# Kernel tuning notes

Measured on AMD Instinct MI355X. Metric: run time of the kernel, lower is better.

The kernel has to match this reference:

```python
import jax, jax.numpy as jnp
import numpy as np

B, N, H = 128, 1024, 128          # graphs, nodes per graph, hidden size
K1, K2, K3 = 512, 256, 128        # ceil(ratio^l * N), ratio = 0.5
DEG = 8                           # avg degree
E = B * N * DEG                   # total edges (fixed, masked after pooling)


def gcn_conv(x, row, col, mask, W, b, n):
    h = x @ W
    deg = jax.ops.segment_sum(mask, col, num_segments=n) + 1.0  # + self loop
    dinv = jax.lax.rsqrt(deg)
    coef = (dinv[row] * dinv[col] * mask)[:, None]
    agg = jax.ops.segment_sum(h[row] * coef, col, num_segments=n)
    return agg + h * (dinv * dinv)[:, None] + b  # self-loop term + bias


def topk_pool(x, row, col, mask, p, n_graphs, n_per, k):
    # PyG TopKPooling: y = x.p/||p||, keep per-graph top-k, x' = x[perm]*tanh(y[perm])
    score = (x @ p) / jnp.linalg.norm(p)
    vals, idx = jax.lax.top_k(score.reshape(n_graphs, n_per), k)  # [B, k]
    sel = (idx + (jnp.arange(n_graphs) * n_per)[:, None]).reshape(-1)
    xs = x[sel] * jnp.tanh(vals.reshape(-1))[:, None]
    # relabel edges; drop edges touching removed nodes via mask
    newid = jnp.full((n_graphs * n_per,), -1, jnp.int32).at[sel].set(
        jnp.arange(n_graphs * k, dtype=jnp.int32))
    nr, nc = newid[row], newid[col]
    nmask = mask * ((nr >= 0) & (nc >= 0)).astype(mask.dtype)
    return xs, jnp.maximum(nr, 0), jnp.maximum(nc, 0), nmask


def readout(x, n_graphs, k):
    # cat([gmp, gap]) with contiguous equal-size graphs
    xg = x.reshape(n_graphs, k, -1)
    return jnp.concatenate([xg.max(axis=1), xg.mean(axis=1)], axis=1)


def _forward(x, edge_row, edge_col, W1, b1, p1, W2, b2, p2, W3, b3, p3):
    mask = jnp.ones((E,), x.dtype)
    h = jax.nn.relu(gcn_conv(x, edge_row, edge_col, mask, W1, b1, B * N))
    x1, r, c, m = topk_pool(h, edge_row, edge_col, mask, p1, B, N, K1)
    out = readout(x1, B, K1)
    h = jax.nn.relu(gcn_conv(x1, r, c, m, W2, b2, B * K1))
    x2, r, c, m = topk_pool(h, r, c, m, p2, B, K1, K2)
    out = out + readout(x2, B, K2)
    h = jax.nn.relu(gcn_conv(x2, r, c, m, W3, b3, B * K2))
    x3, r, c, m = topk_pool(h, r, c, m, p3, B, K2, K3)
    out = out + readout(x3, B, K3)
    return out  # [B, 2*H]


def setup_inputs() -> dict:
    key = jax.random.key(0)
    ks = jax.random.split(key, 12)
    x = jax.random.normal(ks[0], (B * N, H), jnp.float32)
    off = (jnp.arange(B, dtype=jnp.int32) * N)[:, None]
    edge_row = (jax.random.randint(ks[1], (B, N * DEG), 0, N, jnp.int32) + off).reshape(-1)
    edge_col = (jax.random.randint(ks[2], (B, N * DEG), 0, N, jnp.int32) + off).reshape(-1)
    s = 1.0 / np.sqrt(H)
    params = {}
    for i, tag in enumerate(["1", "2", "3"]):
        params["W" + tag] = jax.random.normal(ks[3 + 3 * i], (H, H), jnp.float32) * s
        params["b" + tag] = jnp.zeros((H,), jnp.float32)
        params["p" + tag] = jax.random.normal(ks[4 + 3 * i], (H,), jnp.float32)
    return {"x": x, "edge_row": edge_row, "edge_col": edge_col, **params}


def reference(x, edge_row, edge_col, W1, b1, p1, W2, b2, p2, W3, b3, p3):
    return _forward(x, edge_row, edge_col, W1, b1, p1, W2, b2, p2, W3, b3, p3)
```

## Files before the change

### kernel.cpp

```cpp
#include <hip/hip_runtime.h>
#include <math.h>

#define BG   128
#define NPER 1024
#define HDIM 128
#define NEDGE (BG * NPER * 8)
#define NMAX (BG * NPER)
#define EPG  (NEDGE / BG)
#define CAP  48
#define PRE  16

typedef __attribute__((ext_vector_type(8))) short s16x8;
typedef __attribute__((ext_vector_type(4))) float f32x4;

static __device__ __forceinline__ ushort f2bf(float f) {
  uint u = __float_as_uint(f);
  return (ushort)((u + 0x7fffu + ((u >> 16) & 1u)) >> 16);
}
static __device__ __forceinline__ float bf2f(ushort h) {
  return __uint_as_float(((uint)h) << 16);
}

extern __shared__ float ldsbuf[];


__global__ __launch_bounds__(1024) void countfill_lds_kernel(
    const int* __restrict__ cr, const int* __restrict__ cc,
    int* __restrict__ cnt, int* __restrict__ meta8,
    int* __restrict__ srcext, int* __restrict__ order,
    int* __restrict__ odeg) {
  int* smeta = (int*)ldsbuf;
  int* scnt  = smeta + NPER * PRE;
  int* sbb   = scnt + NPER;
  int g = blockIdx.x, t = threadIdx.x;
  scnt[t] = 0;
  if (t < 2) sbb[t] = 0;
  __syncthreads();

  const int4* cr4 = (const int4*)(cr + (size_t)g * EPG);
  const int4* cc4 = (const int4*)(cc + (size_t)g * EPG);
  #pragma unroll
  for (int i = 0; i < 2; ++i) {
    int4 r = cr4[t * 2 + i];
    int4 c = cc4[t * 2 + i];
    int rl, cl, pos;
    cl = c.x & (NPER - 1); rl = r.x & (NPER - 1);
    pos = atomicAdd(&scnt[cl], 1);
    if (pos < PRE) smeta[cl * PRE + pos] = rl;
    else if (pos < CAP) srcext[((size_t)g * NPER + cl) * CAP + pos] = rl;
    cl = c.y & (NPER - 1); rl = r.y & (NPER - 1);
    pos = atomicAdd(&scnt[cl], 1);
    if (pos < PRE) smeta[cl * PRE + pos] = rl;
    else if (pos < CAP) srcext[((size_t)g * NPER + cl) * CAP + pos] = rl;
    cl = c.z & (NPER - 1); rl = r.z & (NPER - 1);
    pos = atomicAdd(&scnt[cl], 1);
    if (pos < PRE) smeta[cl * PRE + pos] = rl;
    else if (pos < CAP) srcext[((size_t)g * NPER + cl) * CAP + pos] = rl;
    cl = c.w & (NPER - 1); rl = r.w & (NPER - 1);
    pos = atomicAdd(&scnt[cl], 1);
    if (pos < PRE) smeta[cl * PRE + pos] = rl;
    else if (pos < CAP) srcext[((size_t)g * NPER + cl) * CAP + pos] = rl;
  }
  __syncthreads();

  int4* mo = (int4*)(meta8 + (size_t)g * NPER * PRE);
  const int4* sm4 = (const int4*)smeta;
  #pragma unroll
  for (int i = 0; i < 4; ++i) mo[i * 1024 + t] = sm4[i * 1024 + t];
  int d = scnt[t];
  cnt[g * NPER + t] = d;

  int bkt = d > 8 ? 1 : 0;
  int bpos = atomicAdd(&sbb[bkt], 1);
  __syncthreads();
  int slot = bkt ? sbb[0] + bpos : bpos;
  order[g * NPER + slot] = t;
  odeg[g * NPER + slot] = d;
}


__global__ __launch_bounds__(1024) void agg_lds_kernel(
    const float* __restrict__ x, float* __restrict__ z,
    const int* __restrict__ meta8, const int* __restrict__ srcext,
    const int* __restrict__ deg, const int* __restrict__ order,
    const int* __restrict__ odeg, int npg) {
  float* sX = ldsbuf;
  float* sDinv = sX + npg * 32;
  int g = blockIdx.x >> 2;
  int chunk = blockIdx.x & 3;
  int t = threadIdx.x;
  int base = g * npg;

  const float4* x4 = (const float4*)x;
  float4* sX4 = (float4*)sX;
  for (int i = t; i < npg * 8; i += 1024) {
    int r = i >> 3, l8 = i & 7;
    float dv = rsqrtf((float)deg[base + r] + 1.0f);
    float4 v = x4[(size_t)(base + r) * 32 + chunk * 8 + l8];
    v.x *= dv; v.y *= dv; v.z *= dv; v.w *= dv;
    sX4[i] = v;
  }
  for (int i = t; i < npg; i += 1024)
    sDinv[i] = rsqrtf((float)deg[base + i] + 1.0f);

  int dl = t >> 3, l = t & 7;
  const int4* m4 = (const int4*)meta8;
  float4* z4 = (float4*)z;

  int ordc = order[base + dl];
  int dpc  = odeg[base + dl];
  int ordn = order[base + dl + 128];
  int dpn  = odeg[base + dl + 128];
  int4 c0 = m4[(size_t)(base + ordc) * 4 + 0];
  int4 c1 = m4[(size_t)(base + ordc) * 4 + 1];
  int4 c2 = {0, 0, 0, 0}, c3 = {0, 0, 0, 0};
  if (dpc > 8) {
    c2 = m4[(size_t)(base + ordc) * 4 + 2];
    c3 = m4[(size_t)(base + ordc) * 4 + 3];
  }

  __syncthreads();

  for (int slot = dl; slot < npg; slot += 128) {
    int ordn2 = ordn, dpn2 = dpn;
    if (slot + 256 < npg) {
      ordn2 = order[base + slot + 256];
      dpn2  = odeg[base + slot + 256];
    }
    int4 n0 = {0,0,0,0}, n1 = {0,0,0,0}, n2 = {0,0,0,0}, n3 = {0,0,0,0};
    if (slot + 128 < npg) {
      n0 = m4[(size_t)(base + ordn) * 4 + 0];
      n1 = m4[(size_t)(base + ordn) * 4 + 1];
      if (dpn > 8) {
        n2 = m4[(size_t)(base + ordn) * 4 + 2];
        n3 = m4[(size_t)(base + ordn) * 4 + 3];
      }
    }

    int dst = ordc;
    int node = base + dst;
    int d = dpc > CAP ? CAP : dpc;
    int dp = d > PRE ? PRE : d;
    float dc = sDinv[dst];

    int sA0 = (0 < dp) ? c0.x : dst;
    int sA1 = (1 < dp) ? c0.y : dst;
    int sA2 = (2 < dp) ? c0.z : dst;
    int sA3 = (3 < dp) ? c0.w : dst;
    int sA4 = (4 < dp) ? c1.x : dst;
    int sA5 = (5 < dp) ? c1.y : dst;
    int sA6 = (6 < dp) ? c1.z : dst;
    int sA7 = (7 < dp) ? c1.w : dst;
    float4 w  = sX4[dst * 8 + l];
    float4 p0 = sX4[sA0 * 8 + l];
    float4 p1 = sX4[sA1 * 8 + l];
    float4 p2 = sX4[sA2 * 8 + l];
    float4 p3 = sX4[sA3 * 8 + l];
    float4 p4 = sX4[sA4 * 8 + l];
    float4 p5 = sX4[sA5 * 8 + l];
    float4 p6 = sX4[sA6 * 8 + l];
    float4 p7 = sX4[sA7 * 8 + l];
    float4 a0, a1, a2, a3;
    a0.x = w.x + p0.x; a0.y = w.y + p0.y; a0.z = w.z + p0.z; a0.w = w.w + p0.w;
    a1.x = p1.x + p5.x; a1.y = p1.y + p5.y; a1.z = p1.z + p5.z; a1.w = p1.w + p5.w;
    a2.x = p2.x + p6.x; a2.y = p2.y + p6.y; a2.z = p2.z + p6.z; a2.w = p2.w + p6.w;
    a3.x = p3.x + p7.x; a3.y = p3.y + p7.y; a3.z = p3.z + p7.z; a3.w = p3.w + p7.w;
    a0.x += p4.x; a0.y += p4.y; a0.z += p4.z; a0.w += p4.w;

    int nslots = 8;
    if (dp > 8) {
      int sB0 = (8 < dp)  ? c2.x : dst;
      int sB1 = (9 < dp)  ? c2.y : dst;
      int sB2 = (10 < dp) ? c2.z : dst;
      int sB3 = (11 < dp) ? c2.w : dst;
      int sB4 = (12 < dp) ? c3.x : dst;
      int sB5 = (13 < dp) ? c3.y : dst;
      int sB6 = (14 < dp) ? c3.z : dst;
      int sB7 = (15 < dp) ? c3.w : dst;
      float4 q0 = sX4[sB0 * 8 + l];
      float4 q1 = sX4[sB1 * 8 + l];
      float4 q2 = sX4[sB2 * 8 + l];
      float4 q3 = sX4[sB3 * 8 + l];
      float4 q4 = sX4[sB4 * 8 + l];
      float4 q5 = sX4[sB5 * 8 + l];
      float4 q6 = sX4[sB6 * 8 + l];
      float4 q7 = sX4[sB7 * 8 + l];
      a0.x += q0.x; a0.y += q0.y; a0.z += q0.z; a0.w += q0.w;
      a1.x += q1.x; a1.y += q1.y; a1.z += q1.z; a1.w += q1.w;
      a2.x += q2.x; a2.y += q2.y; a2.z += q2.z; a2.w += q2.w;
      a3.x += q3.x; a3.y += q3.y; a3.z += q3.z; a3.w += q3.w;
      a0.x += q4.x; a0.y += q4.y; a0.z += q4.z; a0.w += q4.w;
      a1.x += q5.x; a1.y += q5.y; a1.z += q5.z; a1.w += q5.w;
      a2.x += q6.x; a2.y += q6.y; a2.z += q6.z; a2.w += q6.w;
      a3.x += q7.x; a3.y += q7.y; a3.z += q7.z; a3.w += q7.w;
      nslots = 16;
    }

    if (d > PRE) {
      for (int e2 = PRE; e2 < d; ++e2) {
        int rl = srcext[(size_t)node * CAP + e2];
        float4 v0 = sX4[rl * 8 + l];
        a0.x += v0.x; a0.y += v0.y; a0.z += v0.z; a0.w += v0.w;
      }
    }

    float corr = (float)(nslots - dp);
    float4 o;
    o.x = (a0.x + a1.x + a2.x + a3.x - corr * w.x) * dc;
    o.y = (a0.y + a1.y + a2.y + a3.y - corr * w.y) * dc;
    o.z = (a0.z + a1.z + a2.z + a3.z - corr * w.z) * dc;
    o.w = (a0.w + a1.w + a2.w + a3.w - corr * w.w) * dc;
    z4[(size_t)node * 32 + chunk * 8 + l] = o;

    ordc = ordn; dpc = dpn; ordn = ordn2; dpn = dpn2;
    c0 = n0; c1 = n1; c2 = n2; c3 = n3;
  }
}


__global__ __launch_bounds__(256) void wsplit_kernel(
    const float* __restrict__ W0, const float* __restrict__ W1,
    const float* __restrict__ W2, ushort* __restrict__ wpk) {
  int id = blockIdx.x * 256 + threadIdx.x;
  int L = id >> 14;
  int r = id & 16383;
  int i = r & 7;
  int lane = (r >> 3) & 63;
  int nt = (r >> 9) & 7;
  int kt = (r >> 12) & 3;
  int k = kt * 32 + (lane >> 4) * 8 + i;
  int n = nt * 16 + (lane & 15);
  const float* W = (L == 0) ? W0 : (L == 1) ? W1 : W2;
  float v = W[k * HDIM + n];
  ushort h = f2bf(v);
  float r1 = v - bf2f(h);
  ushort m = f2bf(r1);
  ushort lo = f2bf(r1 - bf2f(m));
  size_t base = (size_t)L * 3 * 16384 + (size_t)r;
  wpk[base] = h;
  wpk[base + 16384] = m;
  wpk[base + 32768] = lo;
}


__global__ __launch_bounds__(256, 2) void conv_mfma_kernel(
    float* __restrict__ zh, const ushort* __restrict__ wpk,
    const float* __restrict__ bias, const float* __restrict__ p,
    float* __restrict__ score) {
  int t = threadIdx.x;
  int wv = t >> 6, l = t & 63;
  int lr = l & 15, lq = l >> 4;
  int arowA = blockIdx.x * 128 + wv * 16 + lr;
  int arowB = arowA + 64;
  const float* zrowA = zh + (size_t)arowA * HDIM + lq * 8;
  const float* zrowB = zh + (size_t)arowB * HDIM + lq * 8;

  s16x8 ahA[4], amA[4], alA[4], ahB[4], amB[4], alB[4];
  #pragma unroll
  for (int kt = 0; kt < 4; ++kt) {
    float4 v0 = ((const float4*)(zrowA + kt * 32))[0];
    float4 v1 = ((const float4*)(zrowA + kt * 32))[1];
    float fA[8] = {v0.x, v0.y, v0.z, v0.w, v1.x, v1.y, v1.z, v1.w};
    float4 u0 = ((const float4*)(zrowB + kt * 32))[0];
    float4 u1 = ((const float4*)(zrowB + kt * 32))[1];
    float fB[8] = {u0.x, u0.y, u0.z, u0.w, u1.x, u1.y, u1.z, u1.w};
    #pragma unroll
    for (int i = 0; i < 8; ++i) {
      ushort h = f2bf(fA[i]);
      float r1 = fA[i] - bf2f(h);
      ushort m = f2bf(r1);
      ushort lo = f2bf(r1 - bf2f(m));
      ahA[kt][i] = (short)h; amA[kt][i] = (short)m; alA[kt][i] = (short)lo;
      h = f2bf(fB[i]);
      r1 = fB[i] - bf2f(h);
      m = f2bf(r1);
      lo = f2bf(r1 - bf2f(m));
      ahB[kt][i] = (short)h; amB[kt][i] = (short)m; alB[kt][i] = (short)lo;
    }
  }

  f32x4 accA[8], accB[8];
  #pragma unroll
  for (int nt = 0; nt < 8; ++nt) { accA[nt] = (f32x4)(0.f); accB[nt] = (f32x4)(0.f); }

  const s16x8* wh = (const s16x8*)wpk;
  const s16x8* wm = wh + 2048;
  const s16x8* wl = wm + 2048;

  #pragma unroll
  for (int kt = 0; kt < 4; ++kt) {
    #pragma unroll
    for (int nt = 0; nt < 8; ++nt) {
      int fi = (kt * 8 + nt) * 64 + l;
      s16x8 bh = wh[fi];
      s16x8 bm = wm[fi];
      s16x8 bl = wl[fi];
      accA[nt] = __builtin_amdgcn_mfma_f32_16x16x32_bf16(ahA[kt], bh, accA[nt], 0, 0, 0);
      accA[nt] = __builtin_amdgcn_mfma_f32_16x16x32_bf16(ahA[kt], bm, accA[nt], 0, 0, 0);
      accA[nt] = __builtin_amdgcn_mfma_f32_16x16x32_bf16(amA[kt], bh, accA[nt], 0, 0, 0);
      accA[nt] = __builtin_amdgcn_mfma_f32_16x16x32_bf16(ahA[kt], bl, accA[nt], 0, 0, 0);
      accA[nt] = __builtin_amdgcn_mfma_f32_16x16x32_bf16(alA[kt], bh, accA[nt], 0, 0, 0);
      accA[nt] = __builtin_amdgcn_mfma_f32_16x16x32_bf16(amA[kt], bm, accA[nt], 0, 0, 0);
      accB[nt] = __builtin_amdgcn_mfma_f32_16x16x32_bf16(ahB[kt], bh, accB[nt], 0, 0, 0);
      accB[nt] = __builtin_amdgcn_mfma_f32_16x16x32_bf16(ahB[kt], bm, accB[nt], 0, 0, 0);
      accB[nt] = __builtin_amdgcn_mfma_f32_16x16x32_bf16(amB[kt], bh, accB[nt], 0, 0, 0);
      accB[nt] = __builtin_amdgcn_mfma_f32_16x16x32_bf16(ahB[kt], bl, accB[nt], 0, 0, 0);
      accB[nt] = __builtin_amdgcn_mfma_f32_16x16x32_bf16(alB[kt], bh, accB[nt], 0, 0, 0);
      accB[nt] = __builtin_amdgcn_mfma_f32_16x16x32_bf16(amB[kt], bm, accB[nt], 0, 0, 0);
    }
  }

  int orowA = blockIdx.x * 128 + wv * 16 + lq * 4;
  int orowB = orowA + 64;
  float partA[4] = {0.f, 0.f, 0.f, 0.f};
  float partB[4] = {0.f, 0.f, 0.f, 0.f};
  #pragma unroll
  for (int nt = 0; nt < 8; ++nt) {
    float bv = bias[nt * 16 + lr];
    float pv = p[nt * 16 + lr];
    #pragma unroll
    for (int j = 0; j < 4; ++j) {
      float hA = fmaxf(accA[nt][j] + bv, 0.f);
      partA[j] += hA * pv;
      zh[(size_t)(orowA + j) * HDIM + nt * 16 + lr] = hA;
      float hB = fmaxf(accB[nt][j] + bv, 0.f);
      partB[j] += hB * pv;
      zh[(size_t)(orowB + j) * HDIM + nt * 16 + lr] = hB;
    }
  }
  #pragma unroll
  for (int j = 0; j < 4; ++j) {
    #pragma unroll
    for (int s = 1; s < 16; s <<= 1) {
      partA[j] += __shfl_xor(partA[j], s);
      partB[j] += __shfl_xor(partB[j], s);
    }
    if (lr == 0) {
      score[orowA + j] = partA[j];
      score[orowB + j] = partB[j];
    }
  }
}


__global__ __launch_bounds__(1024) void topk_mega_kernel(
    const float* __restrict__ score, const float* __restrict__ p,
    const float* __restrict__ h, float* __restrict__ xo,
    const int* __restrict__ in_r, const int* __restrict__ in_c,
    int* __restrict__ out_r, int* __restrict__ out_c,
    int* __restrict__ meta8, int* __restrict__ srcext,
    int* __restrict__ cnt, float* __restrict__ acc,
    int* __restrict__ order, int* __restrict__ odeg,
    float* __restrict__ outf, int P, int K, int L) {
  __shared__ float sv[1024];
  __shared__ int si[1024];
  __shared__ int snew[1024];
  __shared__ int scnt[512];
  __shared__ int bb[2];
  __shared__ float s_pn;
  __shared__ float4 smx[32][32], ssm[32][32];
  int g = blockIdx.x;
  int t = threadIdx.x;

  if (L < 2 && t < 512) scnt[t] = 0;
  if (t < 2) bb[t] = 0;
  snew[t] = -1;
  if (t < 128) { float v = p[t]; sv[t] = v * v; }
  __syncthreads();
  for (int off = 64; off; off >>= 1) {
    if (t < off) sv[t] += sv[t + off];
    __syncthreads();
  }
  if (t == 0) s_pn = sqrtf(sv[0]);
  __syncthreads();
  float pn = s_pn;

  sv[t] = score[(size_t)g * P + t];
  si[t] = t;
  for (int size = 2; size <= P; size <<= 1) {
    for (int stride = size >> 1; stride; stride >>= 1) {
      __syncthreads();
      int j = t ^ stride;
      if (j > t) {
        float a = sv[t], b = sv[j];
        int ia = si[t], ib = si[j];
        bool tFirst = (a > b) || (a == b && ia < ib);
        bool up = ((t & size) == 0);
        if (up ? !tFirst : tFirst) {
          sv[t] = b; sv[j] = a;
          si[t] = ib; si[j] = ia;
        }
      }
    }
  }
  __syncthreads();
  if (t < K) {
    snew[si[t]] = t;
    sv[t] = tanhf(sv[t] / pn);
  }
  __syncthreads();

  int lane = t & 31, grp = t >> 5;
  const float4* h4 = (const float4*)h;
  float4* xo4 = (float4*)xo;
  size_t hbase = (size_t)g * P * 32;
  float4 mx = make_float4(-INFINITY, -INFINITY, -INFINITY, -INFINITY);
  float4 sm = make_float4(0.f, 0.f, 0.f, 0.f);
  #pragma unroll
  for (int i = 0; i < 16; ++i) {
    int j = grp * 16 + i;
    float th = sv[j];
    float4 v = h4[hbase + (size_t)si[j] * 32 + lane];
    v.x *= th; v.y *= th; v.z *= th; v.w *= th;
    xo4[((size_t)g * K + j) * 32 + lane] = v;
    mx.x = fmaxf(mx.x, v.x); mx.y = fmaxf(mx.y, v.y);
    mx.z = fmaxf(mx.z, v.z); mx.w = fmaxf(mx.w, v.w);
    sm.x += v.x; sm.y += v.y; sm.z += v.z; sm.w += v.w;
  }
  smx[grp][lane] = mx;
  ssm[grp][lane] = sm;
  __syncthreads();
  int ngrp = P >> 5;
  if (grp == 0) {
    for (int s2 = 1; s2 < ngrp; ++s2) {
      float4 m2 = smx[s2][lane], s3 = ssm[s2][lane];
      mx.x = fmaxf(mx.x, m2.x); mx.y = fmaxf(mx.y, m2.y);
      mx.z = fmaxf(mx.z, m2.z); mx.w = fmaxf(mx.w, m2.w);
      sm.x += s3.x; sm.y += s3.y; sm.z += s3.z; sm.w += s3.w;
    }
    int c0 = lane * 4;
    if (L < 2) {
      float* amax = acc + (size_t)L * BG * 256 + (size_t)g * 256;
      float* asum = amax + 128;
      amax[c0 + 0] = mx.x; amax[c0 + 1] = mx.y;
      amax[c0 + 2] = mx.z; amax[c0 + 3] = mx.w;
      asum[c0 + 0] = sm.x; asum[c0 + 1] = sm.y;
      asum[c0 + 2] = sm.z; asum[c0 + 3] = sm.w;
    } else {
      sv[c0 + 0] = mx.x; sv[c0 + 1] = mx.y;
      sv[c0 + 2] = mx.z; sv[c0 + 3] = mx.w;
      sv[128 + c0 + 0] = sm.x; sv[128 + c0 + 1] = sm.y;
      sv[128 + c0 + 2] = sm.z; sv[128 + c0 + 3] = sm.w;
    }
  }

  if (L == 2) {
    __syncthreads();
    float v;
    const float* a0 = acc + (size_t)g * 256;
    const float* a1 = acc + (size_t)BG * 256 + (size_t)g * 256;
    if (t < 128) {
      v = a0[t] + a1[t] + sv[t];
    } else {
      v = a0[t] * (1.f / 512.f) + a1[t] * (1.f / 256.f) + sv[t] * (1.f / 128.f);
    }
    outf[g * 256 + t] = v;
    return;
  }

  int ept = EPG / P;
  int ebase = g * EPG;
  for (int i = 0; i < ept; ++i) {
    int e = ebase + i * P + t;
    int r = in_r[e];
    int nr = -1, nc = -1;
    if (r >= 0) {
      nr = snew[r & (P - 1)];
      nc = snew[in_c[e] & (P - 1)];
    }
    bool ok = (nr >= 0) && (nc >= 0);
    out_r[e] = ok ? g * K + nr : -1;
    out_c[e] = ok ? g * K + nc : -1;
    if (ok) {
      int pos = atomicAdd(&scnt[nc], 1);
      size_t gnode = (size_t)g * K + nc;
      if (pos < PRE) {
        meta8[gnode * PRE + pos] = nr;
      } else if (pos < CAP) {
        srcext[gnode * CAP + pos] = nr;
      }
    }
  }
  __syncthreads();
  if (t < K) cnt[g * K + t] = scnt[t];

  int bkt = 0, bpos = 0, bdeg = 0;
  if (t < K) {
    bdeg = scnt[t];
    bkt = bdeg > 8 ? 1 : 0;
    bpos = atomicAdd(&bb[bkt], 1);
  }
  __syncthreads();
  if (t < K) {
    int slot = bkt ? bb[0] + bpos : bpos;
    order[g * K + slot] = t;
    odeg[g * K + slot] = bdeg;
  }
}


extern "C" void kernel_launch(void* const* d_in, const int* in_sizes, int n_in,
                              void* d_out, int out_size, void* d_ws, size_t ws_size,
                              hipStream_t stream) {
  const float* x0 = (const float*)d_in[0];
  const int* erow = (const int*)d_in[1];
  const int* ecol = (const int*)d_in[2];
  const float* Wm[3] = {(const float*)d_in[3], (const float*)d_in[6], (const float*)d_in[9]};
  const float* bm[3] = {(const float*)d_in[4], (const float*)d_in[7], (const float*)d_in[10]};
  const float* pm[3] = {(const float*)d_in[5], (const float*)d_in[8], (const float*)d_in[11]};

  char* w = (char*)d_ws;
  size_t off = 0;
  auto alloc = [&](size_t bytes) -> void* {
    void* ptr = w + off;
    off = (off + bytes + 255) & ~(size_t)255;
    return ptr;
  };
  int* cur_row = (int*)alloc((size_t)NEDGE * 4);
  int* cur_col = (int*)alloc((size_t)NEDGE * 4);
  int* meta8   = (int*)alloc((size_t)NMAX * PRE * 4);
  int* srcext  = (int*)alloc((size_t)NMAX * CAP * 4);
  int* cnt     = (int*)alloc((size_t)NMAX * 4);
  int* order   = (int*)alloc((size_t)NMAX * 4);
  int* odeg    = (int*)alloc((size_t)NMAX * 4);
  float* score = (float*)alloc((size_t)NMAX * 4);
  float* acc   = (float*)alloc((size_t)2 * BG * 256 * 4);
  float* zh    = (float*)alloc((size_t)NMAX * HDIM * 4);
  float* x1    = (float*)alloc((size_t)BG * 512 * HDIM * 4);
  float* x2    = (float*)alloc((size_t)BG * 256 * HDIM * 4);
  float* x3    = (float*)alloc((size_t)BG * 128 * HDIM * 4);
  ushort* wpk  = (ushort*)alloc((size_t)3 * 3 * 16384 * 2);

  hipFuncSetAttribute((const void*)agg_lds_kernel,
                      hipFuncAttributeMaxDynamicSharedMemorySize, 152 * 1024);
  hipFuncSetAttribute((const void*)countfill_lds_kernel,
                      hipFuncAttributeMaxDynamicSharedMemorySize, 72 * 1024);

  size_t cfLds = (size_t)(NPER * PRE + NPER + 2) * 4;
  countfill_lds_kernel<<<BG, 1024, cfLds, stream>>>(
      erow, ecol, cnt, meta8, srcext, order, odeg);
  wsplit_kernel<<<(3 * 16384) / 256, 256, 0, stream>>>(Wm[0], Wm[1], Wm[2], wpk);

  const float* xin = x0;
  float* xout[3] = {x1, x2, x3};
  int Ps[3] = {1024, 512, 256};

  for (int L = 0; L < 3; ++L) {
    int P = Ps[L];
    int K = P >> 1;
    int n = BG * P;
    const int* in_r = (L == 0) ? erow : cur_row;
    const int* in_c = (L == 0) ? ecol : cur_col;
    size_t ldsBytes = (size_t)(P * 33) * 4;

    agg_lds_kernel<<<BG * 4, 1024, ldsBytes, stream>>>(
        xin, zh, meta8, srcext, cnt, order, odeg, P);
    conv_mfma_kernel<<<n / 128, 256, 0, stream>>>(
        zh, wpk + (size_t)L * 3 * 16384, bm[L], pm[L], score);
    topk_mega_kernel<<<BG, P, 0, stream>>>(
        score, pm[L], zh, xout[L], in_r, in_c, cur_row, cur_col,
        meta8, srcext, cnt, acc, order, odeg, (float*)d_out, P, K, L);
    xin = xout[L];
  }
}
```

Baseline: 327.1 us.

## Stage packed weights through double-buffered LDS in conv MFMA kernel

Each k-tile of the packed three-way bf16 weight split is now loaded cooperatively into a double-buffered shared-memory tile, and the next tile's weights and activations are prefetched into registers while the current tile is converted and multiplied. Previously every wave read all weight fragments directly from global memory and held all split activations for four k-tiles in registers. The goal is less redundant global/L2 weight traffic and lower register pressure, which is why the min-blocks launch bound was dropped. The cost is two block barriers per k-tile and 48KB of LDS per block, which may limit occupancy.

New measurement: 317.6 us. 2.9% less time.

```diff
diff --git a/kernel.cpp b/kernel.cpp
--- a/kernel.cpp
+++ b/kernel.cpp
@@ -243,10 +243,11 @@
 }
 
 
-__global__ __launch_bounds__(256, 2) void conv_mfma_kernel(
+__global__ __launch_bounds__(256) void conv_mfma_kernel(
     float* __restrict__ zh, const ushort* __restrict__ wpk,
     const float* __restrict__ bias, const float* __restrict__ p,
     float* __restrict__ score) {
+  __shared__ short sB[2][12288];
   int t = threadIdx.x;
   int wv = t >> 6, l = t & 63;
   int lr = l & 15, lq = l >> 4;
@@ -255,59 +256,90 @@
   const float* zrowA = zh + (size_t)arowA * HDIM + lq * 8;
   const float* zrowB = zh + (size_t)arowB * HDIM + lq * 8;
 
-  s16x8 ahA[4], amA[4], alA[4], ahB[4], amB[4], alB[4];
+  const int4* wp4 = (const int4*)wpk;
+  int i0 = t, i1 = t + 256, i2 = t + 512;
+  int i3 = t + 768, i4 = t + 1024, i5 = t + 1280;
+  int s0 = (i0 >> 9) * 2048 + (i0 & 511);
+  int s1 = (i1 >> 9) * 2048 + (i1 & 511);
+  int s2 = (i2 >> 9) * 2048 + (i2 & 511);
+  int s3 = (i3 >> 9) * 2048 + (i3 & 511);
+  int s4 = (i4 >> 9) * 2048 + (i4 & 511);
+  int s5 = (i5 >> 9) * 2048 + (i5 & 511);
+
+  int4 rg0 = wp4[s0], rg1 = wp4[s1], rg2 = wp4[s2];
+  int4 rg3 = wp4[s3], rg4 = wp4[s4], rg5 = wp4[s5];
+  float4 cA0 = ((const float4*)zrowA)[0];
+  float4 cA1 = ((const float4*)zrowA)[1];
+  float4 cB0 = ((const float4*)zrowB)[0];
+  float4 cB1 = ((const float4*)zrowB)[1];
+  {
+    int4* sw = (int4*)sB[0];
+    sw[i0] = rg0; sw[i1] = rg1; sw[i2] = rg2;
+    sw[i3] = rg3; sw[i4] = rg4; sw[i5] = rg5;
+  }
+  __syncthreads();
+
+  f32x4 accA[8], accB[8];
   #pragma unroll
+  for (int nt = 0; nt < 8; ++nt) { accA[nt] = (f32x4)(0.f); accB[nt] = (f32x4)(0.f); }
+
   for (int kt = 0; kt < 4; ++kt) {
-    float4 v0 = ((const float4*)(zrowA + kt * 32))[0];
-    float4 v1 = ((const float4*)(zrowA + kt * 32))[1];
-    float fA[8] = {v0.x, v0.y, v0.z, v0.w, v1.x, v1.y, v1.z, v1.w};
-    float4 u0 = ((const float4*)(zrowB + kt * 32))[0];
-    float4 u1 = ((const float4*)(zrowB + kt * 32))[1];
-    float fB[8] = {u0.x, u0.y, u0.z, u0.w, u1.x, u1.y, u1.z, u1.w};
+    int cur = kt & 1;
+    float4 nA0, nA1, nB0, nB1;
+    if (kt < 3) {
+      int kb = (kt + 1) * 512;
+      rg0 = wp4[s0 + kb]; rg1 = wp4[s1 + kb]; rg2 = wp4[s2 + kb];
+      rg3 = wp4[s3 + kb]; rg4 = wp4[s4 + kb]; rg5 = wp4[s5 + kb];
+      nA0 = ((const float4*)(zrowA + (kt + 1) * 32))[0];
+      nA1 = ((const float4*)(zrowA + (kt + 1) * 32))[1];
+      nB0 = ((const float4*)(zrowB + (kt + 1) * 32))[0];
+      nB1 = ((const float4*)(zrowB + (kt + 1) * 32))[1];
+    }
+
+    s16x8 ahA, amA, alA, ahB, amB, alB;
+    float fA[8] = {cA0.x, cA0.y, cA0.z, cA0.w, cA1.x, cA1.y, cA1.z, cA1.w};
+    float fB[8] = {cB0.x, cB0.y, cB0.z, cB0.w, cB1.x, cB1.y, cB1.z, cB1.w};
     #pragma unroll
     for (int i = 0; i < 8; ++i) {
       ushort h = f2bf(fA[i]);
       float r1 = fA[i] - bf2f(h);
       ushort m = f2bf(r1);
       ushort lo = f2bf(r1 - bf2f(m));
-      ahA[kt][i] = (short)h; amA[kt][i] = (short)m; alA[kt][i] = (short)lo;
+      ahA[i] = (short)h; amA[i] = (short)m; alA[i] = (short)lo;
       h = f2bf(fB[i]);
       r1 = fB[i] - bf2f(h);
       m = f2bf(r1);
       lo = f2bf(r1 - bf2f(m));
-      ahB[kt][i] = (short)h; amB[kt][i] = (short)m; alB[kt][i] = (short)lo;
-    }
-  }
-
-  f32x4 accA[8], accB[8];
-  #pragma unroll
-  for (int nt = 0; nt < 8; ++nt) { accA[nt] = (f32x4)(0.f); accB[nt] = (f32x4)(0.f); }
-
-  const s16x8* wh = (const s16x8*)wpk;
-  const s16x8* wm = wh + 2048;
-  const s16x8* wl = wm + 2048;
-
-  #pragma unroll
-  for (int kt = 0; kt < 4; ++kt) {
+      ahB[i] = (short)h; amB[i] = (short)m; alB[i] = (short)lo;
+    }
+
+    const s16x8* sb = (const s16x8*)sB[cur];
     #pragma unroll
     for (int nt = 0; nt < 8; ++nt) {
-      int fi = (kt * 8 + nt) * 64 + l;
-      s16x8 bh = wh[fi];
-      s16x8 bm = wm[fi];
-      s16x8 bl = wl[fi];
-      accA[nt] = __builtin_amdgcn_mfma_f32_16x16x32_bf16(ahA[kt], bh, accA[nt], 0, 0, 0);
-      accA[nt] = __builtin_amdgcn_mfma_f32_16x16x32_bf16(ahA[kt], bm, accA[nt], 0, 0, 0);
-      accA[nt] = __builtin_amdgcn_mfma_f32_16x16x32_bf16(amA[kt], bh, accA[nt], 0, 0, 0);
-      accA[nt] = __builtin_amdgcn_mfma_f32_16x16x32_bf16(ahA[kt], bl, accA[nt], 0, 0, 0);
-      accA[nt] = __builtin_amdgcn_mfma_f32_16x16x32_bf16(alA[kt], bh, accA[nt], 0, 0, 0);
-      accA[nt] = __builtin_amdgcn_mfma_f32_16x16x32_bf16(amA[kt], bm, accA[nt], 0, 0, 0);
-      accB[nt] = __builtin_amdgcn_mfma_f32_16x16x32_bf16(ahB[kt], bh, accB[nt], 0, 0, 0);
-      accB[nt] = __builtin_amdgcn_mfma_f32_16x16x32_bf16(ahB[kt], bm, accB[nt], 0, 0, 0);
-      accB[nt] = __builtin_amdgcn_mfma_f32_16x16x32_bf16(amB[kt], bh, accB[nt], 0, 0, 0);
-      accB[nt] = __builtin_amdgcn_mfma_f32_16x16x32_bf16(ahB[kt], bl, accB[nt], 0, 0, 0);
-      accB[nt] = __builtin_amdgcn_mfma_f32_16x16x32_bf16(alB[kt], bh, accB[nt], 0, 0, 0);
-      accB[nt] = __builtin_amdgcn_mfma_f32_16x16x32_bf16(amB[kt], bm, accB[nt], 0, 0, 0);
-    }
+      s16x8 bh = sb[nt * 64 + l];
+      s16x8 bm = sb[512 + nt * 64 + l];
+      s16x8 bl = sb[1024 + nt * 64 + l];
+      accA[nt] = __builtin_amdgcn_mfma_f32_16x16x32_bf16(ahA, bh, accA[nt], 0, 0, 0);
+      accA[nt] = __builtin_amdgcn_mfma_f32_16x16x32_bf16(ahA, bm, accA[nt], 0, 0, 0);
+      accA[nt] = __builtin_amdgcn_mfma_f32_16x16x32_bf16(amA, bh, accA[nt], 0, 0, 0);
+      accA[nt] = __builtin_amdgcn_mfma_f32_16x16x32_bf16(ahA, bl, accA[nt], 0, 0, 0);
+      accA[nt] = __builtin_amdgcn_mfma_f32_16x16x32_bf16(alA, bh, accA[nt], 0, 0, 0);
+      accA[nt] = __builtin_amdgcn_mfma_f32_16x16x32_bf16(amA, bm, accA[nt], 0, 0, 0);
+      accB[nt] = __builtin_amdgcn_mfma_f32_16x16x32_bf16(ahB, bh, accB[nt], 0, 0, 0);
+      accB[nt] = __builtin_amdgcn_mfma_f32_16x16x32_bf16(ahB, bm, accB[nt], 0, 0, 0);
+      accB[nt] = __builtin_amdgcn_mfma_f32_16x16x32_bf16(amB, bh, accB[nt], 0, 0, 0);
+      accB[nt] = __builtin_amdgcn_mfma_f32_16x16x32_bf16(ahB, bl, accB[nt], 0, 0, 0);
+      accB[nt] = __builtin_amdgcn_mfma_f32_16x16x32_bf16(alB, bh, accB[nt], 0, 0, 0);
+      accB[nt] = __builtin_amdgcn_mfma_f32_16x16x32_bf16(amB, bm, accB[nt], 0, 0, 0);
+    }
+    __syncthreads();
+    if (kt < 3) {
+      int4* sw = (int4*)sB[cur ^ 1];
+      sw[i0] = rg0; sw[i1] = rg1; sw[i2] = rg2;
+      sw[i3] = rg3; sw[i4] = rg4; sw[i5] = rg5;
+      cA0 = nA0; cA1 = nA1; cB0 = nB0; cB1 = nB1;
+    }
+    __syncthreads();
   }
 
   int orowA = blockIdx.x * 128 + wv * 16 + lq * 4;
```
